# Kernel tuning notes

Hardware: AMD Instinct MI355X
Metric: run time of the kernel (lower is better)

Reference implementation:

```python
import jax, jax.numpy as jnp
import numpy as np

EPS_POS = 0.65
EPS_NEG = 0.4
TAU = 0.03
TEMPERATURE = 0.07


def setup_inputs() -> dict:
    key = jax.random.key(0)
    k1, k2 = jax.random.split(key)
    N, H, W, C = 256, 14, 14, 512  # ResNet18 layer4 features (448x448 frame), pooled audio
    frame = jax.random.normal(k1, (N, H, W, C), dtype=jnp.float32)
    audio = jax.random.normal(k2, (N, C), dtype=jnp.float32)
    return {"frame": frame, "audio": audio}


def reference(frame, audio):
    # frame: [N, H, W, C] vision backbone features; audio: [N, C] pooled audio embedding
    N = frame.shape[0]
    f = frame * jax.lax.rsqrt(jnp.sum(frame * frame, axis=3, keepdims=True))  # l2_normalize axis=3
    a = audio * jax.lax.rsqrt(jnp.sum(audio * audio, axis=1, keepdims=True))  # l2_normalize axis=1

    # S_ii: per-sample spatial similarity map [N, 1, H, W]
    S_ii = jnp.einsum('nhwc,nc->nhw', f, a)[:, None, :, :]
    # S_ij: cross-batch similarity [N, K, H, W] (K == N)
    S_ij = jnp.einsum('nhwc,kc->nkhw', f, a)

    m_ip = jax.nn.sigmoid((S_ii - EPS_POS) / TAU)   # positive soft-mask
    neg = 1.0 - jax.nn.sigmoid((S_ii - EPS_NEG) / TAU)  # hard-negative soft-mask

    # Pi: masked mean of positive similarities -> [N, 1]
    Pi = jnp.sum(m_ip * S_ii, axis=(2, 3)) / jnp.sum(m_ip, axis=(2, 3))

    n_all = jax.nn.sigmoid((S_ij - EPS_POS) / TAU)
    mask = 1.0 - 100.0 * jnp.eye(N, dtype=frame.dtype)  # kill diagonal (self) pairs
    Ni_easy = (jnp.sum(n_all * S_ij, axis=(2, 3)) / jnp.sum(n_all, axis=(2, 3))) * mask  # [N, N]
    Ni_hard = jnp.sum(neg * S_ii, axis=(2, 3)) / jnp.sum(neg, axis=(2, 3))  # [N, 1]

    data = jnp.concatenate([Pi, Ni_hard, Ni_easy], axis=1) * TEMPERATURE  # [N, N+2]

    # __calc_loss (faithful to TF broadcasting: Pi_d is [N,1], Ni_d is [N] -> [N,N] broadcast)
    Pi_d = data[:, 0:1]
    Ni_d = jnp.sum(data[:, 1:], axis=1)
    Pi_e = jnp.exp(Pi_d)
    Ni_e = jnp.exp(Ni_d)
    loss = (-1.0 / N) * jnp.sum(jnp.log(Pi_e / (Pi_e + Ni_e)))
    return loss
```

## Files before the change

### kernel.cpp

```cpp
#include <hip/hip_runtime.h>
#include <stdint.h>

#define N_IMG 256
#define HW 196
#define CDIM 512

#define F_EPS_POS 0.65f
#define F_EPS_NEG 0.40f
#define F_INV_TAU (1.0f/0.03f)
#define F_TEMP 0.07f

typedef __attribute__((ext_vector_type(8))) short bf16x8;
typedef __attribute__((ext_vector_type(4))) unsigned short u16x4;
typedef __attribute__((ext_vector_type(4))) float f32x4;

__device__ __forceinline__ unsigned short f2bf(float x){
    unsigned int u = __float_as_uint(x);
    u = (u + 0x7FFFu + ((u >> 16) & 1u)) >> 16;
    return (unsigned short)u;
}
__device__ __forceinline__ float sigm(float x){ return 1.0f/(1.0f + __expf(-x)); }

__global__ void audio_norm_k(const float* __restrict__ audio,
                             unsigned short* __restrict__ abf){
    int k = blockIdx.x, t = threadIdx.x;
    __shared__ float red[256];
    float v0 = audio[k*CDIM + t];
    float v1 = audio[k*CDIM + t + 256];
    red[t] = v0*v0 + v1*v1;
    __syncthreads();
    for (int s = 128; s > 0; s >>= 1){
        if (t < s) red[t] += red[t+s];
        __syncthreads();
    }
    float rrt = 1.0f / sqrtf(red[0]);
    abf[k*CDIM + t]       = f2bf(v0*rrt);
    abf[k*CDIM + t + 256] = f2bf(v1*rrt);
}

__global__ __launch_bounds__(512) __attribute__((amdgpu_waves_per_eu(2, 2)))
void main_k(const float* __restrict__ frame,
            const unsigned short* __restrict__ abf,
            float* __restrict__ num, float* __restrict__ den,
            float* __restrict__ hnum, float* __restrict__ hden){
    __shared__ unsigned short fT[2][16*520];
    __shared__ float rnormS[2][16];

    const int t    = threadIdx.x;
    const int n    = blockIdx.x;
    const int lane = t & 63, wid = t >> 6;
    const int col  = lane & 15, quad = lane >> 4;
    const int kg0  = wid*32 + col;
    const int kg1  = kg0 + 16;

    bf16x8 B0[16], B1[16];
    {
        const unsigned short* b0p = abf + (size_t)kg0*CDIM + quad*8;
        const unsigned short* b1p = abf + (size_t)kg1*CDIM + quad*8;
        #pragma unroll
        for (int j = 0; j < 16; ++j){
            B0[j] = *(const bf16x8*)(b0p + j*32);
            B1[j] = *(const bf16x8*)(b1p + j*32);
        }
    }
#define ANCH8(a,b,c,d,e,f,g,h) \
    asm volatile("" : "+v"(a),"+v"(b),"+v"(c),"+v"(d),"+v"(e),"+v"(f),"+v"(g),"+v"(h))
    ANCH8(B0[0],B0[1],B0[2],B0[3],B0[4],B0[5],B0[6],B0[7]);
    ANCH8(B0[8],B0[9],B0[10],B0[11],B0[12],B0[13],B0[14],B0[15]);
    ANCH8(B1[0],B1[1],B1[2],B1[3],B1[4],B1[5],B1[6],B1[7]);
    ANCH8(B1[8],B1[9],B1[10],B1[11],B1[12],B1[13],B1[14],B1[15]);
#undef ANCH8

    const int r0 = 2*wid, r1 = r0 + 1;

    float en0=0.f, en1=0.f, ed0=0.f, ed1=0.f;
    float hn0=0.f, hn1=0.f, hd0=0.f, hd1=0.f;

    const float4* fbase_g = (const float4*)(frame + (size_t)n*HW*CDIM);

    auto loadT = [&](int pt, float4* v){
        int p0 = pt*16 + r0; if (p0 > HW-1) p0 = HW-1;
        int p1 = pt*16 + r1; if (p1 > HW-1) p1 = HW-1;
        const float4* s0 = fbase_g + (size_t)p0*(CDIM/4);
        const float4* s1 = fbase_g + (size_t)p1*(CDIM/4);
        v[0] = s0[lane]; v[1] = s0[lane + 64];
        v[2] = s1[lane]; v[3] = s1[lane + 64];
    };
    auto storeT = [&](const float4* v, int buf){
        float ss0 = v[0].x*v[0].x + v[0].y*v[0].y + v[0].z*v[0].z + v[0].w*v[0].w
                  + v[1].x*v[1].x + v[1].y*v[1].y + v[1].z*v[1].z + v[1].w*v[1].w;
        float ss1 = v[2].x*v[2].x + v[2].y*v[2].y + v[2].z*v[2].z + v[2].w*v[2].w
                  + v[3].x*v[3].x + v[3].y*v[3].y + v[3].z*v[3].z + v[3].w*v[3].w;
        unsigned short* d0 = fT[buf] + r0*520;
        unsigned short* d1 = fT[buf] + r1*520;
        u16x4 u0 = { f2bf(v[0].x), f2bf(v[0].y), f2bf(v[0].z), f2bf(v[0].w) };
        u16x4 u1 = { f2bf(v[1].x), f2bf(v[1].y), f2bf(v[1].z), f2bf(v[1].w) };
        u16x4 u2 = { f2bf(v[2].x), f2bf(v[2].y), f2bf(v[2].z), f2bf(v[2].w) };
        u16x4 u3 = { f2bf(v[3].x), f2bf(v[3].y), f2bf(v[3].z), f2bf(v[3].w) };
        *(u16x4*)(d0 + lane*4)       = u0;
        *(u16x4*)(d0 + 256 + lane*4) = u1;
        *(u16x4*)(d1 + lane*4)       = u2;
        *(u16x4*)(d1 + 256 + lane*4) = u3;
        #pragma unroll
        for (int dd = 1; dd < 64; dd <<= 1){
            ss0 += __shfl_xor(ss0, dd, 64);
            ss1 += __shfl_xor(ss1, dd, 64);
        }
        if (lane == 0){
            rnormS[buf][r0] = (ss0 > 0.f) ? (1.0f/sqrtf(ss0)) : 0.f;
            rnormS[buf][r1] = (ss1 > 0.f) ? (1.0f/sqrtf(ss1)) : 0.f;
        }
    };

    {
        float4 v[4];
        loadT(0, v);
        storeT(v, 0);
    }
    __syncthreads();

    for (int pt = 0; pt < 13; ++pt){
        const int cur = pt & 1, nxt = cur ^ 1;
        const bool hasNext = (pt < 12);

        float4 v[4];
        if (hasNext) loadT(pt + 1, v);

        const unsigned short* fbase = fT[cur] + col*520 + quad*8;
        f32x4 acc0 = {0.f,0.f,0.f,0.f};
        f32x4 acc1 = {0.f,0.f,0.f,0.f};
        #pragma unroll
        for (int j = 0; j < 16; ++j){
            bf16x8 a = *(const bf16x8*)(fbase + j*32);
            acc0 = __builtin_amdgcn_mfma_f32_16x16x32_bf16(a, B0[j], acc0, 0, 0, 0);
            acc1 = __builtin_amdgcn_mfma_f32_16x16x32_bf16(a, B1[j], acc1, 0, 0, 0);
        }
        f32x4 rn4 = *(const f32x4*)(&rnormS[cur][quad*4]);
        #pragma unroll
        for (int rr = 0; rr < 4; ++rr){
            int prow = pt*16 + quad*4 + rr;
            if (prow < HW){
                float s0 = acc0[rr] * rn4[rr];
                float s1 = acc1[rr] * rn4[rr];
                float w0 = sigm((s0 - F_EPS_POS) * F_INV_TAU);
                float w1 = sigm((s1 - F_EPS_POS) * F_INV_TAU);
                en0 += w0*s0; ed0 += w0;
                en1 += w1*s1; ed1 += w1;
                if (kg0 == n){ float wn = 1.f - sigm((s0 - F_EPS_NEG) * F_INV_TAU); hn0 += wn*s0; hd0 += wn; }
                if (kg1 == n){ float wn = 1.f - sigm((s1 - F_EPS_NEG) * F_INV_TAU); hn1 += wn*s1; hd1 += wn; }
            }
        }

        if (hasNext) storeT(v, nxt);
        __syncthreads();
    }

    en0 += __shfl_xor(en0, 16, 64); en0 += __shfl_xor(en0, 32, 64);
    ed0 += __shfl_xor(ed0, 16, 64); ed0 += __shfl_xor(ed0, 32, 64);
    en1 += __shfl_xor(en1, 16, 64); en1 += __shfl_xor(en1, 32, 64);
    ed1 += __shfl_xor(ed1, 16, 64); ed1 += __shfl_xor(ed1, 32, 64);
    hn0 += __shfl_xor(hn0, 16, 64); hn0 += __shfl_xor(hn0, 32, 64);
    hd0 += __shfl_xor(hd0, 16, 64); hd0 += __shfl_xor(hd0, 32, 64);
    hn1 += __shfl_xor(hn1, 16, 64); hn1 += __shfl_xor(hn1, 32, 64);
    hd1 += __shfl_xor(hd1, 16, 64); hd1 += __shfl_xor(hd1, 32, 64);

    if (quad == 0){
        num[n*N_IMG + kg0] = en0;  den[n*N_IMG + kg0] = ed0;
        num[n*N_IMG + kg1] = en1;  den[n*N_IMG + kg1] = ed1;
        if (kg0 == n){ hnum[n] = hn0; hden[n] = hd0; }
        if (kg1 == n){ hnum[n] = hn1; hden[n] = hd1; }
    }
}

__global__ void pd_k(const float* __restrict__ num, const float* __restrict__ den,
                     const float* __restrict__ hnum, const float* __restrict__ hden,
                     float* __restrict__ Pi_d, float* __restrict__ Ni_d){
    int nn = blockIdx.x, t = threadIdx.x;
    __shared__ float red[256];
    __shared__ float diagv;
    float ratio = num[nn*N_IMG + t] / den[nn*N_IMG + t];
    if (t == nn) diagv = ratio;
    red[t] = ratio * (t == nn ? -99.f : 1.f);
    __syncthreads();
    for (int s = 128; s > 0; s >>= 1){
        if (t < s) red[t] += red[t+s];
        __syncthreads();
    }
    if (t == 0){
        Pi_d[nn] = F_TEMP * diagv;
        Ni_d[nn] = F_TEMP * (hnum[nn]/hden[nn] + red[0]);
    }
}

__global__ void loss_k(const float* __restrict__ Pi_d, const float* __restrict__ Ni_d,
                       float* __restrict__ out){
    int i = blockIdx.x, j = threadIdx.x;
    __shared__ float red[256];
    float x = Ni_d[j] - Pi_d[i];
    red[j] = (x > 20.f) ? x : log1pf(__expf(x));
    __syncthreads();
    for (int s = 128; s > 0; s >>= 1){
        if (j < s) red[j] += red[j+s];
        __syncthreads();
    }
    if (j == 0) atomicAdd(out, red[0] * (1.0f/(float)N_IMG));
}

extern "C" void kernel_launch(void* const* d_in, const int* in_sizes, int n_in,
                              void* d_out, int out_size, void* d_ws, size_t ws_size,
                              hipStream_t stream) {
    const float* frame = (const float*)d_in[0];
    const float* audio = (const float*)d_in[1];
    float* out = (float*)d_out;
    char* ws = (char*)d_ws;

    unsigned short* abf = (unsigned short*)(ws);
    float* num  = (float*)(ws + 262144);
    float* den  = (float*)(ws + 524288);
    float* hnum = (float*)(ws + 786432);
    float* hden = (float*)(ws + 787456);
    float* Pi_d = (float*)(ws + 788480);
    float* Ni_d = (float*)(ws + 789504);

    hipMemsetAsync(out, 0, sizeof(float), stream);

    audio_norm_k<<<N_IMG, 256, 0, stream>>>(audio, abf);
    main_k<<<N_IMG, 512, 0, stream>>>(frame, abf, num, den, hnum, hden);
    pd_k<<<N_IMG, 256, 0, stream>>>(num, den, hnum, hden, Pi_d, Ni_d);
    loss_k<<<N_IMG, 256, 0, stream>>>(Pi_d, Ni_d, out);
}
```

Before: 174.5 us.

## Split spatial tiles across blocks and reduce partial sums in pd_k

The main kernel now launches 7×256 blocks, each handling one 32-row spatial tile of one image, instead of 256 blocks that loop serially over 13 tiles. Per-tile partial numerators and denominators go to workspace and are summed in pd_k. The aim is to fill the GPU better, since 256 blocks underuse a 256-CU device and the serial tile loop gives latency-bound behaviour. In exchange, every block reloads the full audio B operand from global memory, the intermediate buffers grow, and the in-block double-buffering is removed.

```diff
diff --git a/kernel.cpp b/kernel.cpp
--- a/kernel.cpp
+++ b/kernel.cpp
@@ -4,6 +4,7 @@
 #define N_IMG 256
 #define HW 196
 #define CDIM 512
+#define NPT 7
 
 #define F_EPS_POS 0.65f
 #define F_EPS_NEG 0.40f
@@ -38,16 +39,17 @@
     abf[k*CDIM + t + 256] = f2bf(v1*rrt);
 }
 
-__global__ __launch_bounds__(512) __attribute__((amdgpu_waves_per_eu(2, 2)))
+__global__ __launch_bounds__(512) __attribute__((amdgpu_waves_per_eu(2)))
 void main_k(const float* __restrict__ frame,
             const unsigned short* __restrict__ abf,
-            float* __restrict__ num, float* __restrict__ den,
-            float* __restrict__ hnum, float* __restrict__ hden){
-    __shared__ unsigned short fT[2][16*520];
-    __shared__ float rnormS[2][16];
+            float* __restrict__ np, float* __restrict__ dp,
+            float* __restrict__ hnp, float* __restrict__ hdp){
+    __shared__ unsigned short A[32*520];
+    __shared__ float rnS[32];
 
     const int t    = threadIdx.x;
-    const int n    = blockIdx.x;
+    const int n    = blockIdx.x & 255;
+    const int pt   = blockIdx.x >> 8;
     const int lane = t & 63, wid = t >> 6;
     const int col  = lane & 15, quad = lane >> 4;
     const int kg0  = wid*32 + col;
@@ -71,77 +73,68 @@
     ANCH8(B1[8],B1[9],B1[10],B1[11],B1[12],B1[13],B1[14],B1[15]);
 #undef ANCH8
 
-    const int r0 = 2*wid, r1 = r0 + 1;
+    {
+        const float4* fbase_g = (const float4*)(frame + (size_t)n*HW*CDIM);
+        float4 v[8];
+        int rr0 = wid*4;
+        #pragma unroll
+        for (int i = 0; i < 4; ++i){
+            int prow = pt*32 + rr0 + i; if (prow > HW-1) prow = HW-1;
+            const float4* s = fbase_g + (size_t)prow*(CDIM/4);
+            v[2*i]   = s[lane];
+            v[2*i+1] = s[lane + 64];
+        }
+        #pragma unroll
+        for (int i = 0; i < 4; ++i){
+            float ss = v[2*i].x*v[2*i].x + v[2*i].y*v[2*i].y
+                     + v[2*i].z*v[2*i].z + v[2*i].w*v[2*i].w
+                     + v[2*i+1].x*v[2*i+1].x + v[2*i+1].y*v[2*i+1].y
+                     + v[2*i+1].z*v[2*i+1].z + v[2*i+1].w*v[2*i+1].w;
+            unsigned short* d = A + (rr0 + i)*520;
+            u16x4 u0 = { f2bf(v[2*i].x),   f2bf(v[2*i].y),
+                         f2bf(v[2*i].z),   f2bf(v[2*i].w) };
+            u16x4 u1 = { f2bf(v[2*i+1].x), f2bf(v[2*i+1].y),
+                         f2bf(v[2*i+1].z), f2bf(v[2*i+1].w) };
+            *(u16x4*)(d + lane*4)       = u0;
+            *(u16x4*)(d + 256 + lane*4) = u1;
+            #pragma unroll
+            for (int dd = 1; dd < 64; dd <<= 1) ss += __shfl_xor(ss, dd, 64);
+            if (lane == 0)
+                rnS[rr0 + i] = (ss > 0.f) ? (1.0f/sqrtf(ss)) : 0.f;
+        }
+    }
+    __syncthreads();
+
+    f32x4 a00 = {0.f,0.f,0.f,0.f}, a01 = {0.f,0.f,0.f,0.f};
+    f32x4 a10 = {0.f,0.f,0.f,0.f}, a11 = {0.f,0.f,0.f,0.f};
+    {
+        const unsigned short* fb0 = A + col*520 + quad*8;
+        const unsigned short* fb1 = A + (16 + col)*520 + quad*8;
+        #pragma unroll
+        for (int j = 0; j < 16; ++j){
+            bf16x8 x0 = *(const bf16x8*)(fb0 + j*32);
+            bf16x8 x1 = *(const bf16x8*)(fb1 + j*32);
+            a00 = __builtin_amdgcn_mfma_f32_16x16x32_bf16(x0, B0[j], a00, 0, 0, 0);
+            a01 = __builtin_amdgcn_mfma_f32_16x16x32_bf16(x0, B1[j], a01, 0, 0, 0);
+            a10 = __builtin_amdgcn_mfma_f32_16x16x32_bf16(x1, B0[j], a10, 0, 0, 0);
+            a11 = __builtin_amdgcn_mfma_f32_16x16x32_bf16(x1, B1[j], a11, 0, 0, 0);
+        }
+    }
 
     float en0=0.f, en1=0.f, ed0=0.f, ed1=0.f;
     float hn0=0.f, hn1=0.f, hd0=0.f, hd1=0.f;
-
-    const float4* fbase_g = (const float4*)(frame + (size_t)n*HW*CDIM);
-
-    auto loadT = [&](int pt, float4* v){
-        int p0 = pt*16 + r0; if (p0 > HW-1) p0 = HW-1;
-        int p1 = pt*16 + r1; if (p1 > HW-1) p1 = HW-1;
-        const float4* s0 = fbase_g + (size_t)p0*(CDIM/4);
-        const float4* s1 = fbase_g + (size_t)p1*(CDIM/4);
-        v[0] = s0[lane]; v[1] = s0[lane + 64];
-        v[2] = s1[lane]; v[3] = s1[lane + 64];
-    };
-    auto storeT = [&](const float4* v, int buf){
-        float ss0 = v[0].x*v[0].x + v[0].y*v[0].y + v[0].z*v[0].z + v[0].w*v[0].w
-                  + v[1].x*v[1].x + v[1].y*v[1].y + v[1].z*v[1].z + v[1].w*v[1].w;
-        float ss1 = v[2].x*v[2].x + v[2].y*v[2].y + v[2].z*v[2].z + v[2].w*v[2].w
-                  + v[3].x*v[3].x + v[3].y*v[3].y + v[3].z*v[3].z + v[3].w*v[3].w;
-        unsigned short* d0 = fT[buf] + r0*520;
-        unsigned short* d1 = fT[buf] + r1*520;
-        u16x4 u0 = { f2bf(v[0].x), f2bf(v[0].y), f2bf(v[0].z), f2bf(v[0].w) };
-        u16x4 u1 = { f2bf(v[1].x), f2bf(v[1].y), f2bf(v[1].z), f2bf(v[1].w) };
-        u16x4 u2 = { f2bf(v[2].x), f2bf(v[2].y), f2bf(v[2].z), f2bf(v[2].w) };
-        u16x4 u3 = { f2bf(v[3].x), f2bf(v[3].y), f2bf(v[3].z), f2bf(v[3].w) };
-        *(u16x4*)(d0 + lane*4)       = u0;
-        *(u16x4*)(d0 + 256 + lane*4) = u1;
-        *(u16x4*)(d1 + lane*4)       = u2;
-        *(u16x4*)(d1 + 256 + lane*4) = u3;
-        #pragma unroll
-        for (int dd = 1; dd < 64; dd <<= 1){
-            ss0 += __shfl_xor(ss0, dd, 64);
-            ss1 += __shfl_xor(ss1, dd, 64);
-        }
-        if (lane == 0){
-            rnormS[buf][r0] = (ss0 > 0.f) ? (1.0f/sqrtf(ss0)) : 0.f;
-            rnormS[buf][r1] = (ss1 > 0.f) ? (1.0f/sqrtf(ss1)) : 0.f;
-        }
-    };
-
-    {
-        float4 v[4];
-        loadT(0, v);
-        storeT(v, 0);
-    }
-    __syncthreads();
-
-    for (int pt = 0; pt < 13; ++pt){
-        const int cur = pt & 1, nxt = cur ^ 1;
-        const bool hasNext = (pt < 12);
-
-        float4 v[4];
-        if (hasNext) loadT(pt + 1, v);
-
-        const unsigned short* fbase = fT[cur] + col*520 + quad*8;
-        f32x4 acc0 = {0.f,0.f,0.f,0.f};
-        f32x4 acc1 = {0.f,0.f,0.f,0.f};
-        #pragma unroll
-        for (int j = 0; j < 16; ++j){
-            bf16x8 a = *(const bf16x8*)(fbase + j*32);
-            acc0 = __builtin_amdgcn_mfma_f32_16x16x32_bf16(a, B0[j], acc0, 0, 0, 0);
-            acc1 = __builtin_amdgcn_mfma_f32_16x16x32_bf16(a, B1[j], acc1, 0, 0, 0);
-        }
-        f32x4 rn4 = *(const f32x4*)(&rnormS[cur][quad*4]);
+    #pragma unroll
+    for (int m = 0; m < 2; ++m){
+        const f32x4& c0 = m ? a10 : a00;
+        const f32x4& c1 = m ? a11 : a01;
         #pragma unroll
         for (int rr = 0; rr < 4; ++rr){
-            int prow = pt*16 + quad*4 + rr;
+            int row  = m*16 + quad*4 + rr;
+            int prow = pt*32 + row;
             if (prow < HW){
-                float s0 = acc0[rr] * rn4[rr];
-                float s1 = acc1[rr] * rn4[rr];
+                float rn = rnS[row];
+                float s0 = c0[rr] * rn;
+                float s1 = c1[rr] * rn;
                 float w0 = sigm((s0 - F_EPS_POS) * F_INV_TAU);
                 float w1 = sigm((s1 - F_EPS_POS) * F_INV_TAU);
                 en0 += w0*s0; ed0 += w0;
@@ -150,9 +143,6 @@
                 if (kg1 == n){ float wn = 1.f - sigm((s1 - F_EPS_NEG) * F_INV_TAU); hn1 += wn*s1; hd1 += wn; }
             }
         }
-
-        if (hasNext) storeT(v, nxt);
-        __syncthreads();
     }
 
     en0 += __shfl_xor(en0, 16, 64); en0 += __shfl_xor(en0, 32, 64);
@@ -165,20 +155,28 @@
     hd1 += __shfl_xor(hd1, 16, 64); hd1 += __shfl_xor(hd1, 32, 64);
 
     if (quad == 0){
-        num[n*N_IMG + kg0] = en0;  den[n*N_IMG + kg0] = ed0;
-        num[n*N_IMG + kg1] = en1;  den[n*N_IMG + kg1] = ed1;
-        if (kg0 == n){ hnum[n] = hn0; hden[n] = hd0; }
-        if (kg1 == n){ hnum[n] = hn1; hden[n] = hd1; }
-    }
-}
-
-__global__ void pd_k(const float* __restrict__ num, const float* __restrict__ den,
-                     const float* __restrict__ hnum, const float* __restrict__ hden,
+        float* npp = np + (size_t)pt*N_IMG*N_IMG + n*N_IMG;
+        float* dpp = dp + (size_t)pt*N_IMG*N_IMG + n*N_IMG;
+        npp[kg0] = en0;  dpp[kg0] = ed0;
+        npp[kg1] = en1;  dpp[kg1] = ed1;
+        if (kg0 == n){ hnp[pt*N_IMG + n] = hn0; hdp[pt*N_IMG + n] = hd0; }
+        if (kg1 == n){ hnp[pt*N_IMG + n] = hn1; hdp[pt*N_IMG + n] = hd1; }
+    }
+}
+
+__global__ void pd_k(const float* __restrict__ np, const float* __restrict__ dp,
+                     const float* __restrict__ hnp, const float* __restrict__ hdp,
                      float* __restrict__ Pi_d, float* __restrict__ Ni_d){
     int nn = blockIdx.x, t = threadIdx.x;
     __shared__ float red[256];
     __shared__ float diagv;
-    float ratio = num[nn*N_IMG + t] / den[nn*N_IMG + t];
+    float nsum = 0.f, dsum = 0.f;
+    #pragma unroll
+    for (int ptile = 0; ptile < NPT; ++ptile){
+        nsum += np[(size_t)ptile*N_IMG*N_IMG + nn*N_IMG + t];
+        dsum += dp[(size_t)ptile*N_IMG*N_IMG + nn*N_IMG + t];
+    }
+    float ratio = nsum / dsum;
     if (t == nn) diagv = ratio;
     red[t] = ratio * (t == nn ? -99.f : 1.f);
     __syncthreads();
@@ -187,8 +185,14 @@
         __syncthreads();
     }
     if (t == 0){
+        float hn = 0.f, hd = 0.f;
+        #pragma unroll
+        for (int ptile = 0; ptile < NPT; ++ptile){
+            hn += hnp[ptile*N_IMG + nn];
+            hd += hdp[ptile*N_IMG + nn];
+        }
         Pi_d[nn] = F_TEMP * diagv;
-        Ni_d[nn] = F_TEMP * (hnum[nn]/hden[nn] + red[0]);
+        Ni_d[nn] = F_TEMP * (hn/hd + red[0]);
     }
 }
 
@@ -215,17 +219,17 @@
     char* ws = (char*)d_ws;
 
     unsigned short* abf = (unsigned short*)(ws);
-    float* num  = (float*)(ws + 262144);
-    float* den  = (float*)(ws + 524288);
-    float* hnum = (float*)(ws + 786432);
-    float* hden = (float*)(ws + 787456);
-    float* Pi_d = (float*)(ws + 788480);
-    float* Ni_d = (float*)(ws + 789504);
+    float* np   = (float*)(ws + 262144);
+    float* dp   = (float*)(ws + 2097152);
+    float* hnp  = (float*)(ws + 3932160);
+    float* hdp  = (float*)(ws + 3940352);
+    float* Pi_d = (float*)(ws + 3948544);
+    float* Ni_d = (float*)(ws + 3949568);
 
     hipMemsetAsync(out, 0, sizeof(float), stream);
 
     audio_norm_k<<<N_IMG, 256, 0, stream>>>(audio, abf);
-    main_k<<<N_IMG, 512, 0, stream>>>(frame, abf, num, den, hnum, hden);
-    pd_k<<<N_IMG, 256, 0, stream>>>(num, den, hnum, hden, Pi_d, Ni_d);
+    main_k<<<NPT*N_IMG, 512, 0, stream>>>(frame, abf, np, dp, hnp, hdp);
+    pd_k<<<N_IMG, 256, 0, stream>>>(np, dp, hnp, hdp, Pi_d, Ni_d);
     loss_k<<<N_IMG, 256, 0, stream>>>(Pi_d, Ni_d, out);
 }
```

Measured after the change: 224.0 us. +28.4%, slower.
